# Performance work log

Hardware: AMD Instinct MI355X
Metric: run time of the kernel (lower is better)

Reference implementation:

```python
import jax, jax.numpy as jnp
import numpy as np

B, S, D = 2, 2048, 2048
H, G, HD = 16, 8, 128          # query heads, kv groups, head_dim
GS = H // G                     # group size (queries per kv head)
EPS = 1e-6


def _rmsnorm(x, scale):
    # Qwen3-compatible: upcast to f32, rms over last dim, scale
    xf = x.astype(jnp.float32)
    ms = jnp.mean(xf * xf, axis=-1, keepdims=True)
    return (xf * jax.lax.rsqrt(ms + EPS) * scale).astype(x.dtype)


def _rope(x, cos, sin):
    # x: (b, h, s, hd); cos/sin: (s, hd) rotate-half convention
    hd = x.shape[-1]
    x1, x2 = x[..., : hd // 2], x[..., hd // 2 :]
    rotated = jnp.concatenate([-x2, x1], axis=-1)
    s = x.shape[2]
    c = cos[None, None, :s, :]
    sn = sin[None, None, :s, :]
    return (x * c + rotated * sn).astype(x.dtype)


def setup_inputs() -> dict:
    key = jax.random.key(0)
    ks = jax.random.split(key, 8)
    x = jax.random.normal(ks[0], (B, S, D), jnp.float32)
    # causal mask: True = masked (future positions)
    mask = jnp.triu(jnp.ones((S, S), dtype=bool), k=1)
    # RoPE tables, rotate-half convention (cat(angles, angles))
    inv_freq = 1.0 / (10000.0 ** (np.arange(0, HD, 2, dtype=np.float32) / HD))
    angles = np.arange(S, dtype=np.float32)[:, None] * inv_freq[None, :]
    angles = np.concatenate([angles, angles], axis=-1)  # (S, HD)
    cos = jnp.asarray(np.cos(angles))
    sin = jnp.asarray(np.sin(angles))
    std = 0.02
    Wq = jax.random.normal(ks[1], (D, H * HD), jnp.float32) * std
    Wk = jax.random.normal(ks[2], (D, G * HD), jnp.float32) * std
    Wv = jax.random.normal(ks[3], (D, G * HD), jnp.float32) * std
    Wo = jax.random.normal(ks[4], (H * HD, D), jnp.float32) * std
    q_scale = jnp.ones((HD,), jnp.float32)
    k_scale = jnp.ones((HD,), jnp.float32)
    return {"x": x, "mask": mask, "cos": cos, "sin": sin,
            "Wq": Wq, "Wk": Wk, "Wv": Wv, "Wo": Wo,
            "q_scale": q_scale, "k_scale": k_scale}


def reference(x, mask, cos, sin, Wq, Wk, Wv, Wo, q_scale, k_scale):
    b, s, _ = x.shape
    q = (x @ Wq).reshape(b, s, H, HD).transpose(0, 2, 1, 3)   # (b,H,s,hd)
    k = (x @ Wk).reshape(b, s, G, HD).transpose(0, 2, 1, 3)   # (b,G,s,hd)
    v = (x @ Wv).reshape(b, s, G, HD).transpose(0, 2, 1, 3)   # (b,G,s,hd)
    q = _rmsnorm(q, q_scale)
    k = _rmsnorm(k, k_scale)
    q = _rope(q, cos, sin)
    k = _rope(k, cos, sin)
    # grouped attention: avoid repeat_interleave by grouping query heads
    qg = q.reshape(b, G, GS, s, HD)
    scores = jnp.einsum('bghqd,bgkd->bghqk', qg, k)           # (b,G,GS,s,s)
    scores = jnp.where(mask[None, None, None, :, :], -jnp.inf, scores)
    weights = jax.nn.softmax(scores / jnp.sqrt(jnp.float32(HD)), axis=-1)
    ctx = jnp.einsum('bghqk,bgkd->bghqd', weights, v)          # (b,G,GS,s,hd)
    ctx = ctx.reshape(b, H, s, HD).transpose(0, 2, 1, 3).reshape(b, s, H * HD)
    return ctx @ Wo
```

## Files before the change

kernel.cpp:

```cpp
#include <hip/hip_runtime.h>
#include <stdint.h>

#define S_LEN 2048
#define NH 16
#define NG 8
#define HDIM 128

typedef __bf16 bf16x8 __attribute__((ext_vector_type(8)));
typedef float f32x4 __attribute__((ext_vector_type(4)));

#define MFMA16(a, b, c) __builtin_amdgcn_mfma_f32_16x16x32_bf16((a), (b), (c), 0, 0, 0)

__device__ __forceinline__ uint16_t f2bf(float f) {
  union { float f; uint32_t u; } v; v.f = f;
  return (uint16_t)((v.u + 0x7fffu + ((v.u >> 16) & 1u)) >> 16);
}

__device__ __forceinline__ void gload16(const void* g, void* l) {
  __builtin_amdgcn_global_load_lds(
      (__attribute__((address_space(1))) const void*)g,
      (__attribute__((address_space(3))) void*)l, 16, 0, 0);
}

__global__ __launch_bounds__(256) void cvt_x_kernel(
    const float* __restrict__ x, uint16_t* __restrict__ xb, int n4) {
  int i = blockIdx.x * 256 + threadIdx.x;
  if (i >= n4) return;
  float4 v = ((const float4*)x)[i];
  ushort4 o;
  o.x = f2bf(v.x); o.y = f2bf(v.y); o.z = f2bf(v.z); o.w = f2bf(v.w);
  ((ushort4*)xb)[i] = o;
}

__global__ __launch_bounds__(256) void trans_cvt_kernel(
    const float* __restrict__ src, uint16_t* __restrict__ dst, int K, int N) {
  __shared__ float T[32][33];
  int n0 = blockIdx.x * 32, k0 = blockIdx.y * 32;
  int tx = threadIdx.x & 31, ty = threadIdx.x >> 5;
  #pragma unroll
  for (int i = 0; i < 4; ++i)
    T[ty + i * 8][tx] = src[(size_t)(k0 + ty + i * 8) * N + n0 + tx];
  __syncthreads();
  #pragma unroll
  for (int i = 0; i < 4; ++i)
    dst[(size_t)(n0 + ty + i * 8) * K + k0 + tx] = f2bf(T[tx][ty + i * 8]);
}

template <int NISSUE>
__device__ __forceinline__ void stage_half(const uint16_t* __restrict__ g,
                                           int ldg, char* lds, int tid) {
  #pragma unroll
  for (int i = 0; i < NISSUE; ++i) {
    int ch = i * 512 + tid;
    int pair = ch >> 3, slotd = ch & 7;
    int slotl = slotd ^ (pair & 7);
    int row = pair * 2 + (slotl >> 2), c2 = slotl & 3;
    gload16(g + (size_t)row * ldg + c2 * 8, lds + ch * 16);
  }
}

__device__ __forceinline__ bf16x8 ldsfrag(const char* half_base, int row, int l4) {
  int pair = row >> 1;
  int slot = ((row & 1) << 2) | l4;
  return *(const bf16x8*)(half_base + pair * 128 + ((slot ^ (pair & 7)) * 16));
}

#define BAR() asm volatile("s_barrier" ::: "memory")

template <int BM>
__global__ __launch_bounds__(512, 2) void gemm8p_kernel(
    const uint16_t* __restrict__ A, const uint16_t* __restrict__ BT,
    float* __restrict__ C, int M, int N, int K, int gridN) {
  extern __shared__ char smem[];
  constexpr int MI = BM / 32;
  constexpr int LA = BM / 128;
  constexpr int ABYTES = BM * 64;
  const int tid = threadIdx.x, lane = tid & 63;
  const int wid = tid >> 6;
  const int l15 = lane & 15, l4 = lane >> 4;
  const int wm = wid >> 2, wn = wid & 3;

  const int nwg = gridDim.x, bid = blockIdx.x;
  const int cpx = nwg >> 3;
  const int swz = (bid & 7) * cpx + (bid >> 3);
  const int m0 = (swz / gridN) * BM, n0 = (swz % gridN) * 256;

  const uint16_t* Ag = A + (size_t)m0 * K;
  const uint16_t* Bg = BT + (size_t)n0 * K;
  const int NT = K >> 6;

#define ABASE(p, k) (smem + (((p) << 1) | (k)) * ABYTES)
#define BBASE(p, k) (smem + 4 * ABYTES + (((p) << 1) | (k)) * 16384)

  f32x4 acc[MI][4];
  #pragma unroll
  for (int mi = 0; mi < MI; ++mi)
    #pragma unroll
    for (int ni = 0; ni < 4; ++ni) acc[mi][ni] = (f32x4){0.f, 0.f, 0.f, 0.f};

  stage_half<LA>(Ag, K, ABASE(0, 0), tid);
  stage_half<2>(Bg, K, BBASE(0, 0), tid);
  stage_half<LA>(Ag + 32, K, ABASE(0, 1), tid);
  stage_half<2>(Bg + 32, K, BBASE(0, 1), tid);
  stage_half<LA>(Ag + 64, K, ABASE(1, 0), tid);
  stage_half<2>(Bg + 64, K, BBASE(1, 0), tid);
  if constexpr (BM == 256) asm volatile("s_waitcnt vmcnt(4)" ::: "memory");
  else                     asm volatile("s_waitcnt vmcnt(3)" ::: "memory");
  BAR();

  int par = 0;
  const int arow = wm * (BM / 2) + l15;
  for (int u = 0; u < NT; ++u, par ^= 1) {
    const int k0 = u * 64;
    bf16x8 af[MI], bf0, bf1;
    #pragma unroll
    for (int mi = 0; mi < MI; ++mi) af[mi] = ldsfrag(ABASE(par, 0), arow + mi * 16, l4);
    bf0 = ldsfrag(BBASE(par, 0), wn * 64 + l15, l4);
    bf1 = ldsfrag(BBASE(par, 0), wn * 64 + 16 + l15, l4);
    if (u + 1 < NT) stage_half<LA>(Ag + (k0 + 96), K, ABASE(par ^ 1, 1), tid);
    BAR();
    __builtin_amdgcn_s_setprio(1);
    #pragma unroll
    for (int mi = 0; mi < MI; ++mi) {
      acc[mi][0] = MFMA16(af[mi], bf0, acc[mi][0]);
      acc[mi][1] = MFMA16(af[mi], bf1, acc[mi][1]);
    }
    __builtin_amdgcn_s_setprio(0);
    BAR();
    bf0 = ldsfrag(BBASE(par, 0), wn * 64 + 32 + l15, l4);
    bf1 = ldsfrag(BBASE(par, 0), wn * 64 + 48 + l15, l4);
    if (u + 1 < NT) stage_half<2>(Bg + (k0 + 96), K, BBASE(par ^ 1, 1), tid);
    BAR();
    __builtin_amdgcn_s_setprio(1);
    #pragma unroll
    for (int mi = 0; mi < MI; ++mi) {
      acc[mi][2] = MFMA16(af[mi], bf0, acc[mi][2]);
      acc[mi][3] = MFMA16(af[mi], bf1, acc[mi][3]);
    }
    __builtin_amdgcn_s_setprio(0);
    BAR();
    #pragma unroll
    for (int mi = 0; mi < MI; ++mi) af[mi] = ldsfrag(ABASE(par, 1), arow + mi * 16, l4);
    bf0 = ldsfrag(BBASE(par, 1), wn * 64 + 32 + l15, l4);
    bf1 = ldsfrag(BBASE(par, 1), wn * 64 + 48 + l15, l4);
    if (u + 2 < NT) stage_half<LA>(Ag + (k0 + 128), K, ABASE(par, 0), tid);
    BAR();
    __builtin_amdgcn_s_setprio(1);
    #pragma unroll
    for (int mi = 0; mi < MI; ++mi) {
      acc[mi][2] = MFMA16(af[mi], bf0, acc[mi][2]);
      acc[mi][3] = MFMA16(af[mi], bf1, acc[mi][3]);
    }
    __builtin_amdgcn_s_setprio(0);
    BAR();
    bf0 = ldsfrag(BBASE(par, 1), wn * 64 + l15, l4);
    bf1 = ldsfrag(BBASE(par, 1), wn * 64 + 16 + l15, l4);
    if (u + 2 < NT) stage_half<2>(Bg + (k0 + 128), K, BBASE(par, 0), tid);
    BAR();
    __builtin_amdgcn_s_setprio(1);
    #pragma unroll
    for (int mi = 0; mi < MI; ++mi) {
      acc[mi][0] = MFMA16(af[mi], bf0, acc[mi][0]);
      acc[mi][1] = MFMA16(af[mi], bf1, acc[mi][1]);
    }
    __builtin_amdgcn_s_setprio(0);
    if (u + 2 < NT) {
      if constexpr (BM == 256) asm volatile("s_waitcnt vmcnt(4)" ::: "memory");
      else                     asm volatile("s_waitcnt vmcnt(3)" ::: "memory");
    } else {
      asm volatile("s_waitcnt vmcnt(0)" ::: "memory");
    }
    BAR();
  }

  #pragma unroll
  for (int mi = 0; mi < MI; ++mi)
    #pragma unroll
    for (int ni = 0; ni < 4; ++ni) {
      float* dst = C + (size_t)(m0 + wm * (BM / 2) + mi * 16 + l4 * 4) * N +
                   n0 + wn * 64 + ni * 16 + l15;
      #pragma unroll
      for (int r = 0; r < 4; ++r) dst[(size_t)r * N] = acc[mi][ni][r];
    }
#undef ABASE
#undef BBASE
}

__global__ __launch_bounds__(256) void qk_rope_kernel(
    const float* __restrict__ QKV, const float* __restrict__ cosb,
    const float* __restrict__ sinb, const float* __restrict__ qs,
    const float* __restrict__ ks, uint16_t* __restrict__ Qb,
    uint16_t* __restrict__ Kb) {
  const int task = blockIdx.x * 4 + (threadIdx.x >> 6);
  const int lane = threadIdx.x & 63;
  const int hh = task % 24;
  const int row = task / 24;
  const int s = row & (S_LEN - 1);
  const int b = row >> 11;
  const float c1 = cosb[s * 128 + lane], c2 = cosb[s * 128 + 64 + lane];
  const float s1 = sinb[s * 128 + lane], s2 = sinb[s * 128 + 64 + lane];
  const float* src = QKV + (size_t)row * 4096;
  float v1, v2, sc1, sc2, outscale;
  uint16_t* dst;
  if (hh < 16) {
    v1 = src[hh * 128 + lane]; v2 = src[hh * 128 + 64 + lane];
    sc1 = qs[lane]; sc2 = qs[lane + 64];
    outscale = 0.088388347648318447f;
    dst = Qb + ((size_t)(b * NH + hh) * S_LEN + s) * 128;
  } else {
    int g = hh - 16;
    v1 = src[2048 + g * 128 + lane]; v2 = src[2048 + g * 128 + 64 + lane];
    sc1 = ks[lane]; sc2 = ks[lane + 64];
    outscale = 1.0f;
    dst = Kb + ((size_t)(b * NG + g) * S_LEN + s) * 128;
  }
  float ss = v1 * v1 + v2 * v2;
  #pragma unroll
  for (int o = 1; o < 64; o <<= 1) ss += __shfl_xor(ss, o);
  float inv = rsqrtf(ss * (1.0f / 128.0f) + 1e-6f);
  float n1 = v1 * inv * sc1, n2 = v2 * inv * sc2;
  dst[lane] = f2bf((n1 * c1 - n2 * s1) * outscale);
  dst[lane + 64] = f2bf((n2 * c2 + n1 * s2) * outscale);
}

__global__ __launch_bounds__(256) void v_trans_kernel(
    const float* __restrict__ QKV, uint16_t* __restrict__ Vt) {
  __shared__ uint16_t T[128][72];
  const int s0 = blockIdx.x * 64;
  const int bg = blockIdx.y;
  const int b = bg >> 3, g = bg & 7;
  const int tid = threadIdx.x;
  const int tc = tid & 127, tr = tid >> 7;
  const float* src = QKV + ((size_t)(b * S_LEN + s0)) * 4096 + 3072 + g * 128;
  #pragma unroll
  for (int i = 0; i < 32; ++i) {
    int r = i * 2 + tr;
    T[tc][r] = f2bf(src[(size_t)r * 4096 + tc]);
  }
  __syncthreads();
  uint16_t* dst = Vt + (size_t)bg * 128 * S_LEN + s0;
  #pragma unroll
  for (int i = 0; i < 32; ++i) {
    int idx = i * 256 + tid;
    int d = idx >> 6, sof = idx & 63;
    dst[(size_t)d * S_LEN + sof] = T[d][sof];
  }
}

__global__ __launch_bounds__(256) void attn_kernel(
    const uint16_t* __restrict__ Qb, const uint16_t* __restrict__ Kb,
    const uint16_t* __restrict__ Vt, uint16_t* __restrict__ Ctx) {
  __shared__ uint8_t smem[65536 + 4 * 2304];
  const int tid = threadIdx.x, lane = tid & 63, wid = tid >> 6;
  uint16_t* Ps = (uint16_t*)(smem + 65536) + wid * 1152;
  const int l15 = lane & 15, l4 = lane >> 4;

  const int bh = blockIdx.y;
  const int b = bh >> 4, h = bh & 15;
  const int bg = b * NG + (h >> 1);

  const uint16_t* Qh = Qb + (size_t)bh * S_LEN * HDIM;
  const uint16_t* Kh = Kb + (size_t)bg * S_LEN * HDIM;
  const uint16_t* Vh = Vt + (size_t)bg * HDIM * S_LEN;

  const int k_row = lane >> 4, k_c = lane & 15;
  const int v_row = lane >> 3, v_c = lane & 7;

#define STAGE(kt_, buf_)                                                      \
  do {                                                                        \
    const int kv0_ = (kt_) * 64;                                              \
    uint16_t* KsB_ = (uint16_t*)(smem + (buf_) * 16384);                      \
    uint16_t* VsB_ = (uint16_t*)(smem + 32768 + (buf_) * 16384);              \
    _Pragma("unroll")                                                         \
    for (int i_ = 0; i_ < 4; ++i_) {                                          \
      int chunk_ = wid * 4 + i_;                                              \
      int row_ = chunk_ * 4 + k_row;                                          \
      int sc_ = (k_c ^ (row_ & 7)) * 8;                                       \
      gload16(Kh + (size_t)(kv0_ + row_) * HDIM + sc_, KsB_ + chunk_ * 512);  \
    }                                                                         \
    _Pragma("unroll")                                                         \
    for (int i_ = 0; i_ < 4; ++i_) {                                          \
      int chunk_ = wid * 4 + i_;                                              \
      int row_ = chunk_ * 8 + v_row;                                          \
      int sc_ = (v_c ^ (row_ & 7)) * 8;                                       \
      gload16(Vh + (size_t)row_ * S_LEN + kv0_ + sc_, VsB_ + chunk_ * 512);   \
    }                                                                         \
  } while (0)

  for (int half = 0; half < 2; ++half) {
    const int qtile = half ? (31 - (int)blockIdx.x) : (int)blockIdx.x;
    const int q0 = qtile * 64;
    const int qrow = q0 + wid * 16 + l15;

    bf16x8 qf[4];
    #pragma unroll
    for (int kk = 0; kk < 4; ++kk)
      qf[kk] = *(const bf16x8*)(Qh + (size_t)qrow * HDIM + kk * 32 + l4 * 8);

    f32x4 acc[8];
    #pragma unroll
    for (int i = 0; i < 8; ++i) acc[i] = (f32x4){0.f, 0.f, 0.f, 0.f};
    float mrun = -1e30f, lrun = 0.f;

    const int nt = qtile + 1;
    int cur = 0;
    STAGE(0, 0);
    asm volatile("s_waitcnt vmcnt(0)\ns_barrier" ::: "memory");

    for (int kt = 0; kt < nt; ++kt) {
      const int kv0 = kt * 64;
      if (kt + 1 < nt) STAGE(kt + 1, cur ^ 1);

      uint16_t* Ks = (uint16_t*)(smem + cur * 16384);
      uint16_t* Vs = (uint16_t*)(smem + 32768 + cur * 16384);

      f32x4 sc[4];
      #pragma unroll
      for (int i = 0; i < 4; ++i) sc[i] = (f32x4){0.f, 0.f, 0.f, 0.f};
      __builtin_amdgcn_s_setprio(1);
      #pragma unroll
      for (int kk = 0; kk < 4; ++kk) {
        #pragma unroll
        for (int kc = 0; kc < 4; ++kc) {
          int key = kc * 16 + l15;
          int cc = (kk * 4 + l4) ^ (key & 7);
          bf16x8 kf = *(const bf16x8*)(Ks + key * 128 + cc * 8);
          sc[kc] = MFMA16(kf, qf[kk], sc[kc]);
        }
      }
      __builtin_amdgcn_s_setprio(0);
      if (kt == nt - 1) {
        #pragma unroll
        for (int kc = 0; kc < 4; ++kc)
          #pragma unroll
          for (int r = 0; r < 4; ++r)
            if (kv0 + kc * 16 + l4 * 4 + r > qrow) sc[kc][r] = -1e30f;
      }
      float tmax = -1e30f;
      #pragma unroll
      for (int kc = 0; kc < 4; ++kc)
        #pragma unroll
        for (int r = 0; r < 4; ++r) tmax = fmaxf(tmax, sc[kc][r]);
      tmax = fmaxf(tmax, __shfl_xor(tmax, 16));
      tmax = fmaxf(tmax, __shfl_xor(tmax, 32));
      float mnew = fmaxf(mrun, tmax);
      float corr = __expf(mrun - mnew);
      float tsum = 0.f;
      #pragma unroll
      for (int kc = 0; kc < 4; ++kc) {
        float p0 = __expf(sc[kc][0] - mnew);
        float p1 = __expf(sc[kc][1] - mnew);
        float p2 = __expf(sc[kc][2] - mnew);
        float p3 = __expf(sc[kc][3] - mnew);
        tsum += (p0 + p1) + (p2 + p3);
        ushort4 pw;
        pw.x = f2bf(p0); pw.y = f2bf(p1); pw.z = f2bf(p2); pw.w = f2bf(p3);
        *(ushort4*)(Ps + l15 * 72 + kc * 16 + l4 * 4) = pw;
      }
      tsum += __shfl_xor(tsum, 16);
      tsum += __shfl_xor(tsum, 32);
      lrun = lrun * corr + tsum;
      mrun = mnew;
      #pragma unroll
      for (int d0 = 0; d0 < 8; ++d0) acc[d0] *= corr;

      __builtin_amdgcn_s_setprio(1);
      #pragma unroll
      for (int hf = 0; hf < 2; ++hf) {
        bf16x8 pf = *(const bf16x8*)(Ps + l15 * 72 + hf * 32 + l4 * 8);
        #pragma unroll
        for (int d0 = 0; d0 < 8; ++d0) {
          int d = d0 * 16 + l15;
          int cc = (hf * 4 + l4) ^ (d & 7);
          bf16x8 vf = *(const bf16x8*)(Vs + d * 64 + cc * 8);
          acc[d0] = MFMA16(vf, pf, acc[d0]);
        }
      }
      __builtin_amdgcn_s_setprio(0);

      asm volatile("s_waitcnt vmcnt(0)\ns_barrier" ::: "memory");
      cur ^= 1;
    }

    float inv = 1.0f / lrun;
    uint16_t* dst = Ctx + ((size_t)(b * S_LEN + qrow) * NH + h) * HDIM;
    #pragma unroll
    for (int d0 = 0; d0 < 8; ++d0) {
      ushort4 o;
      o.x = f2bf(acc[d0][0] * inv);
      o.y = f2bf(acc[d0][1] * inv);
      o.z = f2bf(acc[d0][2] * inv);
      o.w = f2bf(acc[d0][3] * inv);
      *(ushort4*)(dst + d0 * 16 + l4 * 4) = o;
    }
  }
#undef STAGE
}

extern "C" void kernel_launch(void* const* d_in, const int* in_sizes, int n_in,
                              void* d_out, int out_size, void* d_ws, size_t ws_size,
                              hipStream_t stream) {
  const float* x    = (const float*)d_in[0];
  const float* cosb = (const float*)d_in[2];
  const float* sinb = (const float*)d_in[3];
  const float* Wq   = (const float*)d_in[4];
  const float* Wk   = (const float*)d_in[5];
  const float* Wv   = (const float*)d_in[6];
  const float* Wo   = (const float*)d_in[7];
  const float* qs   = (const float*)d_in[8];
  const float* ks   = (const float*)d_in[9];

  char* ws = (char*)d_ws;
  uint16_t* Xb    = (uint16_t*)(ws);
  uint16_t* WallT = (uint16_t*)(ws + (16ull << 20));
  uint16_t* WoT   = (uint16_t*)(ws + (32ull << 20));
  float*    QKV   = (float*)   (ws + (40ull << 20));
  uint16_t* Qb    = (uint16_t*)(ws + (104ull << 20));
  uint16_t* Kb    = (uint16_t*)(ws + (120ull << 20));
  uint16_t* Vt    = (uint16_t*)(ws + (128ull << 20));
  uint16_t* Ctx   = (uint16_t*)(ws + (136ull << 20));
  float* out = (float*)d_out;

  hipFuncSetAttribute(reinterpret_cast<const void*>(&gemm8p_kernel<256>),
                      hipFuncAttributeMaxDynamicSharedMemorySize, 131072);
  hipFuncSetAttribute(reinterpret_cast<const void*>(&gemm8p_kernel<128>),
                      hipFuncAttributeMaxDynamicSharedMemorySize, 98304);

  cvt_x_kernel<<<8192, 256, 0, stream>>>(x, Xb, 2097152);
  trans_cvt_kernel<<<dim3(64, 64), 256, 0, stream>>>(Wq, WallT, 2048, 2048);
  trans_cvt_kernel<<<dim3(32, 64), 256, 0, stream>>>(Wk, WallT + 2048 * 2048, 2048, 1024);
  trans_cvt_kernel<<<dim3(32, 64), 256, 0, stream>>>(Wv, WallT + 3072 * 2048, 2048, 1024);
  trans_cvt_kernel<<<dim3(64, 64), 256, 0, stream>>>(Wo, WoT, 2048, 2048);
  gemm8p_kernel<256><<<256, 512, 131072, stream>>>(Xb, WallT, QKV, 4096, 4096, 2048, 16);
  qk_rope_kernel<<<24576, 256, 0, stream>>>(QKV, cosb, sinb, qs, ks, Qb, Kb);
  v_trans_kernel<<<dim3(32, 16), 256, 0, stream>>>(QKV, Vt);
  attn_kernel<<<dim3(16, 32), 256, 0, stream>>>(Qb, Kb, Vt, Ctx);
  gemm8p_kernel<128><<<256, 512, 98304, stream>>>(Ctx, WoT, out, 4096, 2048, 2048, 8);
}
```

Measured before the change: 358.3 us.

## Share K/V tiles across both GQA heads per block and skip lazy rescales

The attention kernel now launches one 512-thread block per (batch, kv group). Its 8 waves cover both query heads of the group, so each K/V tile staged in LDS is reused by two heads and global K/V traffic is halved. The online softmax now rescales only when the running max rises by more than 8, which removes most exp and accumulator multiplies. bf16 conversion switches to native __bf16 casts. Risks are fewer blocks, which may lower occupancy and worsen tail balance, and a looser max that could lose some precision.

```diff
diff --git a/kernel.cpp b/kernel.cpp
--- a/kernel.cpp
+++ b/kernel.cpp
@@ -7,6 +7,7 @@
 #define HDIM 128
 
 typedef __bf16 bf16x8 __attribute__((ext_vector_type(8)));
+typedef __bf16 bf16x4v __attribute__((ext_vector_type(4)));
 typedef float f32x4 __attribute__((ext_vector_type(4)));
 
 #define MFMA16(a, b, c) __builtin_amdgcn_mfma_f32_16x16x32_bf16((a), (b), (c), 0, 0, 0)
@@ -247,17 +248,18 @@
   }
 }
 
-__global__ __launch_bounds__(256) void attn_kernel(
+__global__ __launch_bounds__(512) void attn_kernel(
     const uint16_t* __restrict__ Qb, const uint16_t* __restrict__ Kb,
     const uint16_t* __restrict__ Vt, uint16_t* __restrict__ Ctx) {
-  __shared__ uint8_t smem[65536 + 4 * 2304];
+  __shared__ uint8_t smem[65536 + 8 * 2304];
   const int tid = threadIdx.x, lane = tid & 63, wid = tid >> 6;
   uint16_t* Ps = (uint16_t*)(smem + 65536) + wid * 1152;
   const int l15 = lane & 15, l4 = lane >> 4;
 
-  const int bh = blockIdx.y;
-  const int b = bh >> 4, h = bh & 15;
-  const int bg = b * NG + (h >> 1);
+  const int bg = blockIdx.y;
+  const int b = bg >> 3, g = bg & 7;
+  const int h = (g << 1) | (wid >> 2);
+  const int bh = b * NH + h;
 
   const uint16_t* Qh = Qb + (size_t)bh * S_LEN * HDIM;
   const uint16_t* Kh = Kb + (size_t)bg * S_LEN * HDIM;
@@ -272,15 +274,15 @@
     uint16_t* KsB_ = (uint16_t*)(smem + (buf_) * 16384);                      \
     uint16_t* VsB_ = (uint16_t*)(smem + 32768 + (buf_) * 16384);              \
     _Pragma("unroll")                                                         \
-    for (int i_ = 0; i_ < 4; ++i_) {                                          \
-      int chunk_ = wid * 4 + i_;                                              \
+    for (int i_ = 0; i_ < 2; ++i_) {                                          \
+      int chunk_ = wid * 2 + i_;                                              \
       int row_ = chunk_ * 4 + k_row;                                          \
       int sc_ = (k_c ^ (row_ & 7)) * 8;                                       \
       gload16(Kh + (size_t)(kv0_ + row_) * HDIM + sc_, KsB_ + chunk_ * 512);  \
     }                                                                         \
     _Pragma("unroll")                                                         \
-    for (int i_ = 0; i_ < 4; ++i_) {                                          \
-      int chunk_ = wid * 4 + i_;                                              \
+    for (int i_ = 0; i_ < 2; ++i_) {                                          \
+      int chunk_ = wid * 2 + i_;                                              \
       int row_ = chunk_ * 8 + v_row;                                          \
       int sc_ = (v_c ^ (row_ & 7)) * 8;                                       \
       gload16(Vh + (size_t)row_ * S_LEN + kv0_ + sc_, VsB_ + chunk_ * 512);   \
@@ -290,7 +292,7 @@
   for (int half = 0; half < 2; ++half) {
     const int qtile = half ? (31 - (int)blockIdx.x) : (int)blockIdx.x;
     const int q0 = qtile * 64;
-    const int qrow = q0 + wid * 16 + l15;
+    const int qrow = q0 + (wid & 3) * 16 + l15;
 
     bf16x8 qf[4];
     #pragma unroll
@@ -343,26 +345,28 @@
         for (int r = 0; r < 4; ++r) tmax = fmaxf(tmax, sc[kc][r]);
       tmax = fmaxf(tmax, __shfl_xor(tmax, 16));
       tmax = fmaxf(tmax, __shfl_xor(tmax, 32));
-      float mnew = fmaxf(mrun, tmax);
-      float corr = __expf(mrun - mnew);
+      if (!__all(tmax <= mrun + 8.0f)) {
+        float mnew = fmaxf(mrun, tmax);
+        float corr = __expf(mrun - mnew);
+        lrun *= corr;
+        #pragma unroll
+        for (int d0 = 0; d0 < 8; ++d0) acc[d0] *= corr;
+        mrun = mnew;
+      }
       float tsum = 0.f;
       #pragma unroll
       for (int kc = 0; kc < 4; ++kc) {
-        float p0 = __expf(sc[kc][0] - mnew);
-        float p1 = __expf(sc[kc][1] - mnew);
-        float p2 = __expf(sc[kc][2] - mnew);
-        float p3 = __expf(sc[kc][3] - mnew);
+        float p0 = __expf(sc[kc][0] - mrun);
+        float p1 = __expf(sc[kc][1] - mrun);
+        float p2 = __expf(sc[kc][2] - mrun);
+        float p3 = __expf(sc[kc][3] - mrun);
         tsum += (p0 + p1) + (p2 + p3);
-        ushort4 pw;
-        pw.x = f2bf(p0); pw.y = f2bf(p1); pw.z = f2bf(p2); pw.w = f2bf(p3);
-        *(ushort4*)(Ps + l15 * 72 + kc * 16 + l4 * 4) = pw;
+        bf16x4v pw = {(__bf16)p0, (__bf16)p1, (__bf16)p2, (__bf16)p3};
+        *(bf16x4v*)(Ps + l15 * 72 + kc * 16 + l4 * 4) = pw;
       }
       tsum += __shfl_xor(tsum, 16);
       tsum += __shfl_xor(tsum, 32);
-      lrun = lrun * corr + tsum;
-      mrun = mnew;
-      #pragma unroll
-      for (int d0 = 0; d0 < 8; ++d0) acc[d0] *= corr;
+      lrun += tsum;
 
       __builtin_amdgcn_s_setprio(1);
       #pragma unroll
@@ -386,12 +390,9 @@
     uint16_t* dst = Ctx + ((size_t)(b * S_LEN + qrow) * NH + h) * HDIM;
     #pragma unroll
     for (int d0 = 0; d0 < 8; ++d0) {
-      ushort4 o;
-      o.x = f2bf(acc[d0][0] * inv);
-      o.y = f2bf(acc[d0][1] * inv);
-      o.z = f2bf(acc[d0][2] * inv);
-      o.w = f2bf(acc[d0][3] * inv);
-      *(ushort4*)(dst + d0 * 16 + l4 * 4) = o;
+      bf16x4v o = {(__bf16)(acc[d0][0] * inv), (__bf16)(acc[d0][1] * inv),
+                   (__bf16)(acc[d0][2] * inv), (__bf16)(acc[d0][3] * inv)};
+      *(bf16x4v*)(dst + d0 * 16 + l4 * 4) = o;
     }
   }
 #undef STAGE
@@ -434,6 +435,6 @@
   gemm8p_kernel<256><<<256, 512, 131072, stream>>>(Xb, WallT, QKV, 4096, 4096, 2048, 16);
   qk_rope_kernel<<<24576, 256, 0, stream>>>(QKV, cosb, sinb, qs, ks, Qb, Kb);
   v_trans_kernel<<<dim3(32, 16), 256, 0, stream>>>(QKV, Vt);
-  attn_kernel<<<dim3(16, 32), 256, 0, stream>>>(Qb, Kb, Vt, Ctx);
+  attn_kernel<<<dim3(16, 16), 512, 0, stream>>>(Qb, Kb, Vt, Ctx);
   gemm8p_kernel<128><<<256, 512, 98304, stream>>>(Ctx, WoT, out, 4096, 2048, 2048, 8);
 }
```

After: 341.8 us. 4.6% less time.
